# Optimization experiments

Measured on AMD Instinct MI355X. Metric: run time of the kernel, lower is better.

The kernel has to match this reference:

```python
import jax, jax.numpy as jnp
import numpy as np

REMAIN_BIT = 12
GROUP_SIZE = 256


def _get_exponent(x):
    # floor(log2(|x| + 1e-30)) as in the torch module
    return jnp.floor(jnp.log2(jnp.abs(x) + 1e-30))


def setup_inputs() -> dict:
    key = jax.random.key(0)
    x = jax.random.normal(key, (4, 4096, 4096), dtype=jnp.float32)
    return {"x": x}


def reference(x) -> jnp.ndarray:
    original_shape = x.shape
    num_groups = original_shape[-1] // GROUP_SIZE
    xg = x.reshape(*original_shape[:-1], num_groups, GROUP_SIZE)

    exp = _get_exponent(xg)                      # [..., G, gs]
    max_exp = jnp.max(exp, axis=-1)              # [..., G]

    # align_and_truncate
    signs = jnp.sign(xg)
    x_abs = jnp.abs(xg)
    e = _get_exponent(x_abs)
    mantissa = x_abs / jnp.exp2(e)
    shift_bits = max_exp[..., None] - e          # >= 0 by construction
    aligned = mantissa * jnp.exp2(-shift_bits)
    truncate_bits = REMAIN_BIT - 2
    scale = jnp.float32(2.0 ** truncate_bits)
    aligned = jnp.floor(aligned * scale) / scale
    result = signs * aligned * jnp.exp2(max_exp[..., None])

    return result.reshape(original_shape)
```

## Files before the change

### kernel.cpp

```cpp
#include <hip/hip_runtime.h>
#include <math.h>


constexpr int GROUP_SIZE = 256;
constexpr int WAVES_PER_BLOCK = 4;

__global__ __launch_bounds__(256, 4)
void align_quant_kernel(const float* __restrict__ x,
                        float* __restrict__ out,
                        int num_groups) {
    const int wave = threadIdx.x >> 6;
    const int lane = threadIdx.x & 63;
    const long long g = (long long)blockIdx.x * WAVES_PER_BLOCK + wave;
    if (g >= num_groups) return;

    const size_t base = (size_t)g * GROUP_SIZE + (size_t)lane * 4;

    const float4 v = *reinterpret_cast<const float4*>(x + base);

    const float a0 = fabsf(v.x), a1 = fabsf(v.y), a2 = fabsf(v.z), a3 = fabsf(v.w);

    const float e0 = floorf(log2f(a0 + 1e-30f));
    const float e1 = floorf(log2f(a1 + 1e-30f));
    const float e2 = floorf(log2f(a2 + 1e-30f));
    const float e3 = floorf(log2f(a3 + 1e-30f));

    float m = fmaxf(fmaxf(e0, e1), fmaxf(e2, e3));
    #pragma unroll
    for (int off = 32; off > 0; off >>= 1)
        m = fmaxf(m, __shfl_xor(m, off, 64));

    const int Mi = (int)m;

    float4 r;
    {
        const int ei = (int)e0;
        const float mant = ldexpf(a0, -ei);
        const float fl = floorf(ldexpf(mant, ei - Mi + 10));
        r.x = copysignf(ldexpf(fl, Mi - 10), v.x);
    }
    {
        const int ei = (int)e1;
        const float mant = ldexpf(a1, -ei);
        const float fl = floorf(ldexpf(mant, ei - Mi + 10));
        r.y = copysignf(ldexpf(fl, Mi - 10), v.y);
    }
    {
        const int ei = (int)e2;
        const float mant = ldexpf(a2, -ei);
        const float fl = floorf(ldexpf(mant, ei - Mi + 10));
        r.z = copysignf(ldexpf(fl, Mi - 10), v.z);
    }
    {
        const int ei = (int)e3;
        const float mant = ldexpf(a3, -ei);
        const float fl = floorf(ldexpf(mant, ei - Mi + 10));
        r.w = copysignf(ldexpf(fl, Mi - 10), v.w);
    }

    *reinterpret_cast<float4*>(out + base) = r;
}

extern "C" void kernel_launch(void* const* d_in, const int* in_sizes, int n_in,
                              void* d_out, int out_size, void* d_ws, size_t ws_size,
                              hipStream_t stream) {
    const float* x = (const float*)d_in[0];
    float* out = (float*)d_out;

    const long long n = (long long)in_sizes[0];
    const int num_groups = (int)(n / GROUP_SIZE);
    const int blocks = (num_groups + WAVES_PER_BLOCK - 1) / WAVES_PER_BLOCK;

    align_quant_kernel<<<blocks, 256, 0, stream>>>(x, out, num_groups);
}
```

Measured before the change: 410.7 us.

## Use nontemporal vector loads/stores and simplify per-element quantization math

Loads and stores now use nontemporal builtins on a native vector type, so the streaming data bypasses cache retention. The per-element mantissa normalization is folded into one scale by 2^(10-max_exp), then floor, then scale back, which removes the intermediate ldexp and exponent casts. The occupancy hint is raised to 8 blocks per CU, and the group index is computed in 32-bit. The folded scaling should be exact for powers of two, but denormal edge cases could differ slightly.

```diff
diff --git a/kernel.cpp b/kernel.cpp
--- a/kernel.cpp
+++ b/kernel.cpp
@@ -5,18 +5,21 @@
 constexpr int GROUP_SIZE = 256;
 constexpr int WAVES_PER_BLOCK = 4;
 
-__global__ __launch_bounds__(256, 4)
+typedef float f32x4 __attribute__((ext_vector_type(4)));
+
+__global__ __launch_bounds__(256, 8)
 void align_quant_kernel(const float* __restrict__ x,
                         float* __restrict__ out,
                         int num_groups) {
     const int wave = threadIdx.x >> 6;
     const int lane = threadIdx.x & 63;
-    const long long g = (long long)blockIdx.x * WAVES_PER_BLOCK + wave;
+    const int g = blockIdx.x * WAVES_PER_BLOCK + wave;
     if (g >= num_groups) return;
 
     const size_t base = (size_t)g * GROUP_SIZE + (size_t)lane * 4;
 
-    const float4 v = *reinterpret_cast<const float4*>(x + base);
+    const f32x4 v = __builtin_nontemporal_load(
+        reinterpret_cast<const f32x4*>(x + base));
 
     const float a0 = fabsf(v.x), a1 = fabsf(v.y), a2 = fabsf(v.z), a3 = fabsf(v.w);
 
@@ -30,35 +33,15 @@
     for (int off = 32; off > 0; off >>= 1)
         m = fmaxf(m, __shfl_xor(m, off, 64));
 
-    const int Mi = (int)m;
+    const int sh = 10 - (int)m;
 
-    float4 r;
-    {
-        const int ei = (int)e0;
-        const float mant = ldexpf(a0, -ei);
-        const float fl = floorf(ldexpf(mant, ei - Mi + 10));
-        r.x = copysignf(ldexpf(fl, Mi - 10), v.x);
-    }
-    {
-        const int ei = (int)e1;
-        const float mant = ldexpf(a1, -ei);
-        const float fl = floorf(ldexpf(mant, ei - Mi + 10));
-        r.y = copysignf(ldexpf(fl, Mi - 10), v.y);
-    }
-    {
-        const int ei = (int)e2;
-        const float mant = ldexpf(a2, -ei);
-        const float fl = floorf(ldexpf(mant, ei - Mi + 10));
-        r.z = copysignf(ldexpf(fl, Mi - 10), v.z);
-    }
-    {
-        const int ei = (int)e3;
-        const float mant = ldexpf(a3, -ei);
-        const float fl = floorf(ldexpf(mant, ei - Mi + 10));
-        r.w = copysignf(ldexpf(fl, Mi - 10), v.w);
-    }
+    f32x4 r;
+    r.x = copysignf(ldexpf(floorf(ldexpf(a0, sh)), -sh), v.x);
+    r.y = copysignf(ldexpf(floorf(ldexpf(a1, sh)), -sh), v.y);
+    r.z = copysignf(ldexpf(floorf(ldexpf(a2, sh)), -sh), v.z);
+    r.w = copysignf(ldexpf(floorf(ldexpf(a3, sh)), -sh), v.w);
 
-    *reinterpret_cast<float4*>(out + base) = r;
+    __builtin_nontemporal_store(r, reinterpret_cast<f32x4*>(out + base));
 }
 
 extern "C" void kernel_launch(void* const* d_in, const int* in_sizes, int n_in,
```

Result: no change. 408.2 us (-0.6%).
